# Kernel tuning notes

Hardware: AMD Instinct MI355X
Metric: run time of the kernel (lower is better)

## Reference

```python
import jax, jax.numpy as jnp
import numpy as np

B, S, D, H = 2, 2048, 1024, 16
DK = D // H


def setup_inputs() -> dict:
    key = jax.random.key(0)
    ks = jax.random.split(key, 12)
    scale = 0.02
    inp = {
        "query": jax.random.normal(ks[0], (B, S, D), jnp.float32),
        "key": jax.random.normal(ks[1], (B, S, D), jnp.float32),
        "value": jax.random.normal(ks[2], (B, S, D), jnp.float32),
        "mask": jax.random.randint(ks[3], (B, S), 0, 2, jnp.int32),
        "Wq": jax.random.normal(ks[4], (D, D), jnp.float32) * scale,
        "bq": jnp.zeros((D,), jnp.float32),
        "Wk": jax.random.normal(ks[5], (D, D), jnp.float32) * scale,
        "bk": jnp.zeros((D,), jnp.float32),
        "Wv": jax.random.normal(ks[6], (D, D), jnp.float32) * scale,
        "bv": jnp.zeros((D,), jnp.float32),
        "Wo": jax.random.normal(ks[7], (D, D), jnp.float32) * scale,
        "bo": jnp.zeros((D,), jnp.float32),
    }
    return inp


def reference(query, key, value, mask, Wq, bq, Wk, bk, Wv, bv, Wo, bo):
    # Linear projections then split heads: [B, S, D] -> [B, H, S, DK]
    def proj(x, W, b):
        y = x @ W.T + b  # torch nn.Linear: x @ W^T + b
        return y.reshape(B, S, H, DK).transpose(0, 2, 1, 3)

    q = proj(query, Wq, bq)
    k = proj(key, Wk, bk)
    v = proj(value, Wv, bv)

    # Scaled dot-product attention with full [B, H, S, S] scores (naive form)
    scores = jnp.einsum("bhqd,bhkd->bhqk", q, k) / jnp.sqrt(jnp.float32(DK))
    # mask==1 marks padding over key positions; broadcast [B,1,1,S]
    pad = (mask == 1)[:, None, None, :]
    scores = jnp.where(pad, -jnp.inf, scores)
    p_attn = jax.nn.softmax(scores, axis=-1)
    # dropout omitted (eval / deterministic mode)
    x = jnp.einsum("bhqk,bhkd->bhqd", p_attn, v)
    x = x.transpose(0, 2, 1, 3).reshape(B, S, D)
    return x @ Wo.T + bo
```

## Files before the change

kernel.cpp:

```cpp
#include <hip/hip_runtime.h>
#include <stdint.h>

typedef short bf16x8 __attribute__((ext_vector_type(8)));
typedef float f32x4  __attribute__((ext_vector_type(4)));
typedef unsigned short u16;

#define BB 2
#define SS 2048
#define DD 1024
#define HH 16
#define NTOK (BB*SS)
#define QSC 0.18033688f

__device__ __forceinline__ u16 f2bf(float f) {
  union { float f; uint32_t u; } c; c.f = f;
  uint32_t r = c.u + 0x7FFFu + ((c.u >> 16) & 1u);
  return (u16)(r >> 16);
}

__device__ __forceinline__ void gll16(const void* g, void* l) {
  __builtin_amdgcn_global_load_lds((__attribute__((address_space(1))) void*)(void*)g,
                                   (__attribute__((address_space(3))) void*)l, 16, 0, 0);
}

struct CvtArgs { const float* src[4]; u16* dst[4]; int n; };
__global__ void cvtn_kernel(CvtArgs a) {
  const float* __restrict__ src = a.src[blockIdx.z];
  u16* __restrict__ dst = a.dst[blockIdx.z];
  int i = (blockIdx.x * blockDim.x + threadIdx.x) * 4;
  const int stride = gridDim.x * blockDim.x * 4;
  for (; i < a.n; i += stride) {
    float4 v = *(const float4*)(src + i);
    ushort4 o;
    o.x = f2bf(v.x); o.y = f2bf(v.y); o.z = f2bf(v.z); o.w = f2bf(v.w);
    *(ushort4*)(dst + i) = o;
  }
}

__global__ __launch_bounds__(256) void maskcnt_kernel(const int* __restrict__ mask,
                                                      float* __restrict__ out) {
  const int b = blockIdx.x, t = threadIdx.x;
  const int4 v1 = *(const int4*)(mask + b * SS + t * 8);
  const int4 v2 = *(const int4*)(mask + b * SS + t * 8 + 4);
  int s = v1.x + v1.y + v1.z + v1.w + v2.x + v2.y + v2.z + v2.w;
#pragma unroll
  for (int off = 32; off; off >>= 1) s += __shfl_xor(s, off);
  __shared__ int red[4];
  if ((t & 63) == 0) red[t >> 6] = s;
  __syncthreads();
  if (t == 0) out[b] = (float)(red[0] + red[1] + red[2] + red[3]);
}

template<int MODE>
__device__ __forceinline__ void gemm_bt_body(const u16* __restrict__ A,
                                             const u16* __restrict__ W,
                                             const float* __restrict__ bias,
                                             const int* __restrict__ mask,
                                             void* __restrict__ Cout) {
  __shared__ __align__(16) u16 As[128 * 32];
  __shared__ __align__(16) u16 Bs[128 * 32];
  const int tid = threadIdx.x;
  const int lane = tid & 63, wid = tid >> 6;
  const int r16 = lane & 15, g4 = lane >> 4;
  const int m0 = blockIdx.y * 128, n0 = blockIdx.x * 128;
  const int wm = (wid >> 1) * 64, wn = (wid & 1) * 64;

  const f32x4 zero = {0.f, 0.f, 0.f, 0.f};
  f32x4 acc[4][4];
#pragma unroll
  for (int i = 0; i < 4; ++i)
#pragma unroll
    for (int j = 0; j < 4; ++j) acc[i][j] = zero;

  const int row0 = tid >> 2, blk0 = tid & 3;
  for (int k0 = 0; k0 < DD; k0 += 32) {
#pragma unroll
    for (int it = 0; it < 2; ++it) {
      const int row = row0 + it * 64;
      const int sb = blk0 ^ (row & 3);
      gll16(A + (size_t)(m0 + row) * DD + k0 + sb * 8, As + (tid + it * 256) * 8);
      gll16(W + (size_t)(n0 + row) * DD + k0 + sb * 8, Bs + (tid + it * 256) * 8);
    }
    __syncthreads();
    bf16x8 af[4], bfr[4];
#pragma unroll
    for (int i = 0; i < 4; ++i) {
      const int ar = wm + i * 16 + r16;
      af[i] = *(const bf16x8*)(As + ar * 32 + ((g4 ^ (ar & 3)) << 3));
      const int br = wn + i * 16 + r16;
      bfr[i] = *(const bf16x8*)(Bs + br * 32 + ((g4 ^ (br & 3)) << 3));
    }
#pragma unroll
    for (int i = 0; i < 4; ++i)
#pragma unroll
      for (int j = 0; j < 4; ++j)
        acc[i][j] = __builtin_amdgcn_mfma_f32_16x16x32_bf16(af[i], bfr[j], acc[i][j], 0, 0, 0);
    __syncthreads();
  }

  float bcol[4];
#pragma unroll
  for (int j = 0; j < 4; ++j) bcol[j] = bias[n0 + wn + j * 16 + r16];

#pragma unroll
  for (int i = 0; i < 4; ++i) {
    const int rowb = m0 + wm + i * 16 + g4 * 4;
    int mr[4] = {0, 0, 0, 0};
    if (MODE == 1 || MODE == 2) {
      const int4 mv = *(const int4*)(mask + rowb);
      mr[0] = mv.x; mr[1] = mv.y; mr[2] = mv.z; mr[3] = mv.w;
    }
#pragma unroll
    for (int j = 0; j < 4; ++j) {
      const int col = n0 + wn + j * 16 + r16;
      if (MODE == 3) {
#pragma unroll
        for (int r = 0; r < 4; ++r)
          ((float*)Cout)[(size_t)(rowb + r) * DD + col] = acc[i][j][r] + bcol[j];
      } else if (MODE == 0) {
#pragma unroll
        for (int r = 0; r < 4; ++r)
          ((u16*)Cout)[(size_t)(rowb + r) * DD + col] = f2bf((acc[i][j][r] + bcol[j]) * QSC);
      } else if (MODE == 1) {
#pragma unroll
        for (int r = 0; r < 4; ++r) {
          const float v = mr[r] ? 0.f : (acc[i][j][r] + bcol[j]);
          ((u16*)Cout)[(size_t)(rowb + r) * DD + col] = f2bf(v);
        }
      } else {
        const int bb = rowb >> 11, s0 = rowb & (SS - 1);
        ushort4 pk;
        pk.x = f2bf(mr[0] ? 0.f : (acc[i][j][0] + bcol[j]));
        pk.y = f2bf(mr[1] ? 0.f : (acc[i][j][1] + bcol[j]));
        pk.z = f2bf(mr[2] ? 0.f : (acc[i][j][2] + bcol[j]));
        pk.w = f2bf(mr[3] ? 0.f : (acc[i][j][3] + bcol[j]));
        *(ushort4*)((u16*)Cout + (size_t)(bb * DD + col) * SS + s0) = pk;
      }
    }
  }
}

struct QkvArgs {
  const u16* A[3];
  const u16* W[3];
  const float* bias[3];
  const int* mask;
  u16* outq; u16* outk; u16* outv;
};

__global__ __launch_bounds__(256) void gemm_qkv_kernel(QkvArgs a) {
  const int z = blockIdx.z;
  if (z == 0)      gemm_bt_body<0>(a.A[0], a.W[0], a.bias[0], nullptr, (void*)a.outq);
  else if (z == 1) gemm_bt_body<1>(a.A[1], a.W[1], a.bias[1], a.mask, (void*)a.outk);
  else             gemm_bt_body<2>(a.A[2], a.W[2], a.bias[2], a.mask, (void*)a.outv);
}

__global__ __launch_bounds__(256) void gemm_out_kernel(const u16* __restrict__ A,
                                                       const u16* __restrict__ W,
                                                       const float* __restrict__ bias,
                                                       float* __restrict__ C) {
  gemm_bt_body<3>(A, W, bias, nullptr, (void*)C);
}

__global__ __launch_bounds__(256) void attn_kernel(const u16* __restrict__ Qp,
                                                   const u16* __restrict__ Kp,
                                                   const u16* __restrict__ Vt,
                                                   const float* __restrict__ padcnt,
                                                   u16* __restrict__ ctx) {
  __shared__ __align__(16) u16 Ks[2][64 * 64];
  __shared__ __align__(16) u16 Vs[2][64 * 64];
  __shared__ __align__(16) uint32_t Ps[4][16 * 32];

  const int tid = threadIdx.x;
  const int lane = tid & 63, wid = tid >> 6;
  const int r16 = lane & 15, g4 = lane >> 4;
  const int qt = blockIdx.x, h = blockIdx.y, b = blockIdx.z;

  const int qtok = b * SS + qt * 64 + wid * 16 + r16;
  bf16x8 qf[2];
#pragma unroll
  for (int c = 0; c < 2; ++c)
    qf[c] = *(const bf16x8*)(Qp + (size_t)qtok * DD + h * 64 + c * 32 + g4 * 8);

  const f32x4 zero = {0.f, 0.f, 0.f, 0.f};
  f32x4 o[4];
#pragma unroll
  for (int j = 0; j < 4; ++j) o[j] = zero;
  float ll = 0.f;

  const int srow0 = tid >> 3, sblk0 = tid & 7;
  const u16* Kbase = Kp + (size_t)(b * SS) * DD + h * 64;
  const u16* Vbase = Vt + (size_t)(b * DD + h * 64) * SS;

  auto stage = [&](int kt, int buf) {
#pragma unroll
    for (int it = 0; it < 2; ++it) {
      const int row = srow0 + it * 32;
      const int sb = sblk0 ^ (row & 7);
      gll16(Kbase + (size_t)(kt * 64 + row) * DD + sb * 8, &Ks[buf][(tid + it * 256) * 8]);
      gll16(Vbase + (size_t)row * SS + kt * 64 + sb * 8, &Vs[buf][(tid + it * 256) * 8]);
    }
  };

  stage(0, 0);
  __syncthreads();

  for (int kt = 0; kt < SS / 64; ++kt) {
    const int cur = kt & 1;
    if (kt + 1 < SS / 64) stage(kt + 1, cur ^ 1);

    f32x4 st[4];
#pragma unroll
    for (int j = 0; j < 4; ++j) st[j] = zero;
#pragma unroll
    for (int c = 0; c < 2; ++c)
#pragma unroll
      for (int j = 0; j < 4; ++j) {
        const int kr = j * 16 + r16;
        const bf16x8 kf = *(const bf16x8*)(&Ks[cur][kr * 64 + (((c * 4 + g4) ^ (kr & 7)) << 3)]);
        st[j] = __builtin_amdgcn_mfma_f32_16x16x32_bf16(kf, qf[c], st[j], 0, 0, 0);
      }

    uint32_t pk[4][2];
#pragma unroll
    for (int j = 0; j < 4; ++j) {
      float p0, p1, p2, p3;
      asm("v_exp_f32 %0, %1" : "=v"(p0) : "v"(st[j][0]));
      asm("v_exp_f32 %0, %1" : "=v"(p1) : "v"(st[j][1]));
      asm("v_exp_f32 %0, %1" : "=v"(p2) : "v"(st[j][2]));
      asm("v_exp_f32 %0, %1" : "=v"(p3) : "v"(st[j][3]));
      ll += (p0 + p1) + (p2 + p3);
      asm("v_cvt_pk_bf16_f32 %0, %1, %2" : "=v"(pk[j][0]) : "v"(p0), "v"(p1));
      asm("v_cvt_pk_bf16_f32 %0, %1, %2" : "=v"(pk[j][1]) : "v"(p2), "v"(p3));
    }

    uint32_t* pw = &Ps[wid][0];
    const int swz = (r16 & 7) << 2;
#pragma unroll
    for (int j = 0; j < 4; ++j) {
      pw[r16 * 32 + ((j * 8 + g4 * 2) ^ swz)] = pk[j][0];
      pw[r16 * 32 + ((j * 8 + g4 * 2 + 1) ^ swz)] = pk[j][1];
    }
    asm volatile("s_waitcnt lgkmcnt(0)" ::: "memory");
    __builtin_amdgcn_sched_barrier(0);

    bf16x8 pa[2];
#pragma unroll
    for (int c = 0; c < 2; ++c)
      pa[c] = *(const bf16x8*)(pw + r16 * 32 + (((c * 16 + g4 * 4)) ^ swz));

#pragma unroll
    for (int c = 0; c < 2; ++c)
#pragma unroll
      for (int j = 0; j < 4; ++j) {
        const int vr = j * 16 + r16;
        const bf16x8 vf = *(const bf16x8*)(&Vs[cur][vr * 64 + (((c * 4 + g4) ^ (vr & 7)) << 3)]);
        o[j] = __builtin_amdgcn_mfma_f32_16x16x32_bf16(pa[c], vf, o[j], 0, 0, 0);
      }
    __syncthreads();
  }

  ll += __shfl_xor(ll, 16);
  ll += __shfl_xor(ll, 32);
  ll -= padcnt[b];
  const float inv = 1.0f / ll;
  float invr[4];
#pragma unroll
  for (int r = 0; r < 4; ++r) invr[r] = __shfl(inv, g4 * 4 + r);

  const int otok = b * SS + qt * 64 + wid * 16 + g4 * 4;
#pragma unroll
  for (int j = 0; j < 4; ++j) {
    const int col = h * 64 + j * 16 + r16;
#pragma unroll
    for (int r = 0; r < 4; ++r)
      ctx[(size_t)(otok + r) * DD + col] = f2bf(o[j][r] * invr[r]);
  }
}

extern "C" void kernel_launch(void* const* d_in, const int* in_sizes, int n_in,
                              void* d_out, int out_size, void* d_ws, size_t ws_size,
                              hipStream_t stream) {
  (void)in_sizes; (void)n_in; (void)out_size; (void)ws_size;
  const float* f_q = (const float*)d_in[0];
  const float* f_k = (const float*)d_in[1];
  const float* f_v = (const float*)d_in[2];
  const int* mask  = (const int*)d_in[3];
  const float* Wq = (const float*)d_in[4];
  const float* bq = (const float*)d_in[5];
  const float* Wk = (const float*)d_in[6];
  const float* bk = (const float*)d_in[7];
  const float* Wv = (const float*)d_in[8];
  const float* bv = (const float*)d_in[9];
  const float* Wo = (const float*)d_in[10];
  const float* bo = (const float*)d_in[11];

  char* ws = (char*)d_ws;
  const size_t XB = (size_t)NTOK * DD * 2;
  const size_t WB = (size_t)DD * DD * 2;
  u16* Xq  = (u16*)(ws);
  u16* Xk  = (u16*)(ws + XB);
  u16* Xv  = (u16*)(ws + 2 * XB);
  u16* Qp  = (u16*)(ws + 3 * XB);
  u16* Kp  = (u16*)(ws + 4 * XB);
  u16* Vt  = (u16*)(ws + 5 * XB);
  u16* Wqb = (u16*)(ws + 6 * XB);
  u16* Wkb = (u16*)(ws + 6 * XB + WB);
  u16* Wvb = (u16*)(ws + 6 * XB + 2 * WB);
  u16* Wob = (u16*)(ws + 6 * XB + 3 * WB);
  float* padcnt = (float*)(ws + 6 * XB + 4 * WB);
  u16* ctx = Xq;

  CvtArgs cx;
  cx.src[0] = f_q; cx.src[1] = f_k; cx.src[2] = f_v; cx.src[3] = f_q;
  cx.dst[0] = Xq;  cx.dst[1] = Xk;  cx.dst[2] = Xv;  cx.dst[3] = Xq;
  cx.n = NTOK * DD;
  cvtn_kernel<<<dim3(1024, 1, 3), 256, 0, stream>>>(cx);

  CvtArgs cw;
  cw.src[0] = Wq;  cw.src[1] = Wk;  cw.src[2] = Wv;  cw.src[3] = Wo;
  cw.dst[0] = Wqb; cw.dst[1] = Wkb; cw.dst[2] = Wvb; cw.dst[3] = Wob;
  cw.n = DD * DD;
  cvtn_kernel<<<dim3(256, 1, 4), 256, 0, stream>>>(cw);

  maskcnt_kernel<<<BB, 256, 0, stream>>>(mask, padcnt);

  QkvArgs qa;
  qa.A[0] = Xq;  qa.A[1] = Xk;  qa.A[2] = Xv;
  qa.W[0] = Wqb; qa.W[1] = Wkb; qa.W[2] = Wvb;
  qa.bias[0] = bq; qa.bias[1] = bk; qa.bias[2] = bv;
  qa.mask = mask;
  qa.outq = Qp; qa.outk = Kp; qa.outv = Vt;
  gemm_qkv_kernel<<<dim3(DD / 128, NTOK / 128, 3), 256, 0, stream>>>(qa);

  attn_kernel<<<dim3(SS / 64, HH, BB), 256, 0, stream>>>(Qp, Kp, Vt, padcnt, ctx);
  gemm_out_kernel<<<dim3(DD / 128, NTOK / 128), 256, 0, stream>>>(ctx, Wob, bo, (float*)d_out);
}
```

Measured before the change: 155.9 us.

## Double-buffer GEMM LDS tiles and use permlane swaps for P relayout

The projection GEMM now double-buffers its A/B LDS tiles, prefetching the next K slice while the current one feeds the MFMAs. This removes one of the two barriers per iteration and hides global-load latency. In attention, the P-matrix round trip through LDS (store, wait, reload) is replaced by permlane32/permlane16 swaps that rearrange the packed bf16 probabilities between lanes in registers. This doubles GEMM LDS use and depends on the permlane lane mapping matching the old LDS layout exactly.

```diff
diff --git a/kernel.cpp b/kernel.cpp
--- a/kernel.cpp
+++ b/kernel.cpp
@@ -3,6 +3,7 @@
 
 typedef short bf16x8 __attribute__((ext_vector_type(8)));
 typedef float f32x4  __attribute__((ext_vector_type(4)));
+typedef unsigned int u32x2 __attribute__((ext_vector_type(2)));
 typedef unsigned short u16;
 
 #define BB 2
@@ -57,8 +58,8 @@
                                              const float* __restrict__ bias,
                                              const int* __restrict__ mask,
                                              void* __restrict__ Cout) {
-  __shared__ __align__(16) u16 As[128 * 32];
-  __shared__ __align__(16) u16 Bs[128 * 32];
+  __shared__ __align__(16) u16 As[2][128 * 32];
+  __shared__ __align__(16) u16 Bs[2][128 * 32];
   const int tid = threadIdx.x;
   const int lane = tid & 63, wid = tid >> 6;
   const int r16 = lane & 15, g4 = lane >> 4;
@@ -73,22 +74,30 @@
     for (int j = 0; j < 4; ++j) acc[i][j] = zero;
 
   const int row0 = tid >> 2, blk0 = tid & 3;
-  for (int k0 = 0; k0 < DD; k0 += 32) {
+  auto stage = [&](int kt, int buf) {
 #pragma unroll
     for (int it = 0; it < 2; ++it) {
       const int row = row0 + it * 64;
       const int sb = blk0 ^ (row & 3);
-      gll16(A + (size_t)(m0 + row) * DD + k0 + sb * 8, As + (tid + it * 256) * 8);
-      gll16(W + (size_t)(n0 + row) * DD + k0 + sb * 8, Bs + (tid + it * 256) * 8);
-    }
-    __syncthreads();
+      gll16(A + (size_t)(m0 + row) * DD + kt * 32 + sb * 8, &As[buf][(tid + it * 256) * 8]);
+      gll16(W + (size_t)(n0 + row) * DD + kt * 32 + sb * 8, &Bs[buf][(tid + it * 256) * 8]);
+    }
+  };
+
+  stage(0, 0);
+  __syncthreads();
+
+  for (int kt = 0; kt < DD / 32; ++kt) {
+    const int cur = kt & 1;
+    if (kt + 1 < DD / 32) stage(kt + 1, cur ^ 1);
+
     bf16x8 af[4], bfr[4];
 #pragma unroll
     for (int i = 0; i < 4; ++i) {
       const int ar = wm + i * 16 + r16;
-      af[i] = *(const bf16x8*)(As + ar * 32 + ((g4 ^ (ar & 3)) << 3));
+      af[i] = *(const bf16x8*)(&As[cur][ar * 32 + ((g4 ^ (ar & 3)) << 3)]);
       const int br = wn + i * 16 + r16;
-      bfr[i] = *(const bf16x8*)(Bs + br * 32 + ((g4 ^ (br & 3)) << 3));
+      bfr[i] = *(const bf16x8*)(&Bs[cur][br * 32 + ((g4 ^ (br & 3)) << 3)]);
     }
 #pragma unroll
     for (int i = 0; i < 4; ++i)
@@ -169,7 +178,6 @@
                                                    u16* __restrict__ ctx) {
   __shared__ __align__(16) u16 Ks[2][64 * 64];
   __shared__ __align__(16) u16 Vs[2][64 * 64];
-  __shared__ __align__(16) uint32_t Ps[4][16 * 32];
 
   const int tid = threadIdx.x;
   const int lane = tid & 63, wid = tid >> 6;
@@ -221,7 +229,7 @@
         st[j] = __builtin_amdgcn_mfma_f32_16x16x32_bf16(kf, qf[c], st[j], 0, 0, 0);
       }
 
-    uint32_t pk[4][2];
+    uint32_t q0[4], q1[4];
 #pragma unroll
     for (int j = 0; j < 4; ++j) {
       float p0, p1, p2, p3;
@@ -230,24 +238,21 @@
       asm("v_exp_f32 %0, %1" : "=v"(p2) : "v"(st[j][2]));
       asm("v_exp_f32 %0, %1" : "=v"(p3) : "v"(st[j][3]));
       ll += (p0 + p1) + (p2 + p3);
-      asm("v_cvt_pk_bf16_f32 %0, %1, %2" : "=v"(pk[j][0]) : "v"(p0), "v"(p1));
-      asm("v_cvt_pk_bf16_f32 %0, %1, %2" : "=v"(pk[j][1]) : "v"(p2), "v"(p3));
-    }
-
-    uint32_t* pw = &Ps[wid][0];
-    const int swz = (r16 & 7) << 2;
-#pragma unroll
-    for (int j = 0; j < 4; ++j) {
-      pw[r16 * 32 + ((j * 8 + g4 * 2) ^ swz)] = pk[j][0];
-      pw[r16 * 32 + ((j * 8 + g4 * 2 + 1) ^ swz)] = pk[j][1];
-    }
-    asm volatile("s_waitcnt lgkmcnt(0)" ::: "memory");
-    __builtin_amdgcn_sched_barrier(0);
+      asm("v_cvt_pk_bf16_f32 %0, %1, %2" : "=v"(q0[j]) : "v"(p0), "v"(p1));
+      asm("v_cvt_pk_bf16_f32 %0, %1, %2" : "=v"(q1[j]) : "v"(p2), "v"(p3));
+    }
 
     bf16x8 pa[2];
 #pragma unroll
-    for (int c = 0; c < 2; ++c)
-      pa[c] = *(const bf16x8*)(pw + r16 * 32 + (((c * 16 + g4 * 4)) ^ swz));
+    for (int c = 0; c < 2; ++c) {
+      u32x2 s0 = __builtin_amdgcn_permlane32_swap(q0[2 * c], q0[2 * c + 1], false, false);
+      u32x2 s1 = __builtin_amdgcn_permlane16_swap(s0.x, s0.y, false, false);
+      u32x2 t0 = __builtin_amdgcn_permlane32_swap(q1[2 * c], q1[2 * c + 1], false, false);
+      u32x2 t1 = __builtin_amdgcn_permlane16_swap(t0.x, t0.y, false, false);
+      union { uint32_t u[4]; bf16x8 v; } cv;
+      cv.u[0] = s1.x; cv.u[1] = t1.x; cv.u[2] = s1.y; cv.u[3] = t1.y;
+      pa[c] = cv.v;
+    }
 
 #pragma unroll
     for (int c = 0; c < 2; ++c)
```

New measurement: 181.4 us. 1.16x slower.
